# Performance work log

Hardware: AMD Instinct MI355X
Metric: run time of the kernel (lower is better)

## Reference

```python
import jax, jax.numpy as jnp
import numpy as np

N_TASKS = 32
SCALING = 32.0 / 16.0  # lora_alpha / r


def setup_inputs() -> dict:
    key = jax.random.key(0)
    k = jax.random.split(key, 6)
    B_, D_IN, D_OUT, R = 32768, 1024, 1024, 16
    x = jax.random.normal(k[0], (B_, D_IN), dtype=jnp.float32)
    task_ids = jax.random.randint(k[1], (B_,), 0, N_TASKS, dtype=jnp.int32)
    W_base = jax.random.normal(k[2], (D_OUT, D_IN), dtype=jnp.float32) * 0.02
    b_base = jax.random.normal(k[3], (D_OUT,), dtype=jnp.float32) * 0.02
    A = jax.random.normal(k[4], (N_TASKS, R, D_IN), dtype=jnp.float32) * 0.02
    B = jax.random.normal(k[5], (N_TASKS, D_OUT, R), dtype=jnp.float32) * 0.02
    return {"x": x, "task_ids": task_ids, "W_base": W_base, "b_base": b_base, "A": A, "B": B}


def reference(x, task_ids, W_base, b_base, A, B):
    # Base linear: [B, D_in] @ [D_in, D_out] + bias
    result = x @ W_base.T + b_base
    # Per-example task routing. Equivalent to gathering A[t], B[t] per row,
    # expressed as a masked dense contraction over the small task axis.
    onehot = jax.nn.one_hot(task_ids, N_TASKS, dtype=x.dtype)  # [B, T]
    # down-projection for every task, then mask to the selected task: [B, T, r]
    ax = jnp.einsum('bi,tri->btr', x, A) * onehot[:, :, None]
    # up-projection contracting out the task axis: [B, D_out]
    lora_out = jnp.einsum('btr,tor->bo', ax, B) * SCALING
    return result + lora_out
```

## Files before the change

kernel.cpp:

```cpp
#include <hip/hip_runtime.h>


#define D_IN   1024
#define D_OUTV 1024
#define NTASK  32
#define NROWS  32768
#define RLORA  16
#define SCALE  2.0f

typedef unsigned short u16;
typedef __attribute__((ext_vector_type(4))) unsigned short u16x4;
typedef __attribute__((ext_vector_type(8))) unsigned short u16x8;
typedef __attribute__((ext_vector_type(8))) short s16x8;
typedef __attribute__((ext_vector_type(4))) float f32x4;

#define WB_OFF   (0)
#define AB_OFF   (2*1024*1024)
#define BB_OFF   (3*1024*1024)
#define CNT_OFF  (4*1024*1024)
#define RIDX_OFF (CNT_OFF + 512)
#define XG_OFF   (8ull*1024*1024)

__device__ __forceinline__ u16 f2bf(float f) {
  union { float f; unsigned u; } v; v.f = f;
  unsigned r = v.u + 0x7fffu + ((v.u >> 16) & 1u);
  return (u16)(r >> 16);
}

__device__ __forceinline__ void gl2lds16(const void* g, void* s) {
  __builtin_amdgcn_global_load_lds(
      (const __attribute__((address_space(1))) unsigned*)g,
      (__attribute__((address_space(3))) unsigned*)s, 16, 0, 0);
}

__global__ void k_convert(const float* __restrict__ W, const float* __restrict__ A,
                          const float* __restrict__ B, u16* __restrict__ Wb,
                          u16* __restrict__ Ab, u16* __restrict__ Bb) {
  int g = blockIdx.x * blockDim.x + threadIdx.x;
  const int NW = D_OUTV * D_IN / 4;
  const int NA = NTASK * RLORA * D_IN / 4;
  const float* src; u16* dst; int idx;
  if (g < NW) { src = W; dst = Wb; idx = g; }
  else if (g < NW + NA) { src = A; dst = Ab; idx = g - NW; }
  else { src = B; dst = Bb; idx = g - NW - NA; }
  f32x4 v = *(const f32x4*)(src + (size_t)idx * 4);
  u16x4 o;
  o[0] = f2bf(v[0]); o[1] = f2bf(v[1]); o[2] = f2bf(v[2]); o[3] = f2bf(v[3]);
  *(u16x4*)(dst + (size_t)idx * 4) = o;
}

__global__ void k_hist(const int* __restrict__ tasks, int* __restrict__ cnt) {
  __shared__ int h[NTASK];
  int tid = threadIdx.x;
  if (tid < NTASK) h[tid] = 0;
  __syncthreads();
  atomicAdd(&h[tasks[blockIdx.x * 256 + tid]], 1);
  __syncthreads();
  if (tid < NTASK) atomicAdd(&cnt[tid], h[tid]);
}

__global__ void k_scan(int* __restrict__ cnt) {
  int t = threadIdx.x;
  int c = (t < NTASK) ? cnt[t] : 0;
  int v = c;
  for (int d = 1; d < NTASK; d <<= 1) {
    int u = __shfl_up(v, d, 64);
    if (t >= d) v += u;
  }
  if (t < NTASK) {
    int ex = v - c;
    cnt[64 + t] = ex;
    cnt[32 + t] = ex;
    if (t == NTASK - 1) cnt[64 + NTASK] = v;
  }
}

__global__ void k_scatter(const int* __restrict__ tasks, int* __restrict__ cnt,
                          int* __restrict__ ridx) {
  __shared__ int h[NTASK], basev[NTASK];
  int tid = threadIdx.x;
  int b = blockIdx.x * 256 + tid;
  int t = tasks[b];
  if (tid < NTASK) h[tid] = 0;
  __syncthreads();
  atomicAdd(&h[t], 1);
  __syncthreads();
  if (tid < NTASK) {
    basev[tid] = atomicAdd(&cnt[32 + tid], h[tid]);
    h[tid] = 0;
  }
  __syncthreads();
  int r = atomicAdd(&h[t], 1);
  ridx[basev[t] + r] = b;
}

__global__ void k_gatherx(const float* __restrict__ x, const int* __restrict__ ridx,
                          u16* __restrict__ xg) {
  int g = blockIdx.x * 256 + threadIdx.x;
  int pos = g >> 7;
  int c8  = (g & 127) << 3;
  int src = ridx[pos];
  f32x4 a = *(const f32x4*)(x + (size_t)src * D_IN + c8);
  f32x4 b = *(const f32x4*)(x + (size_t)src * D_IN + c8 + 4);
  u16x8 o;
  o[0] = f2bf(a[0]); o[1] = f2bf(a[1]); o[2] = f2bf(a[2]); o[3] = f2bf(a[3]);
  o[4] = f2bf(b[0]); o[5] = f2bf(b[1]); o[6] = f2bf(b[2]); o[7] = f2bf(b[3]);
  *(u16x8*)(xg + (size_t)pos * D_IN + c8) = o;
}

#define BM 128
#define BN 128
#define BK 64
#define NTHR 256
#define SLOTS 3
#define NWG (8 * NTASK * SLOTS)

__global__ __launch_bounds__(NTHR, 3) void k_main_c(
    const u16* __restrict__ xg, const float* __restrict__ bias,
    const u16* __restrict__ Wb, const u16* __restrict__ Ab, const u16* __restrict__ Bb,
    const int* __restrict__ cnt, const int* __restrict__ ridx,
    float* __restrict__ out) {
  __shared__ __align__(16) u16 xs[BM * BK];
  __shared__ __align__(16) u16 wls[BN * BK];
  __shared__ u16 als[RLORA * BK];
  __shared__ u16 axs[BM * 32];
  __shared__ u16 bls[BN * 32];
  __shared__ int rowid_l[BM];

  const int tid = threadIdx.x;
  const int l   = tid & 63;
  const int w   = tid >> 6;
  const int wr  = w >> 1;
  const int wc  = w & 1;
  const int l15 = l & 15;
  const int lg  = l >> 4;

  const int flat = blockIdx.x;
  const int xcd  = flat & 7;
  const int j    = flat >> 3;
  const int cb   = j & 7;
  const int g    = j >> 3;
  const int task = xcd + 8 * (g & 3);
  const int slot = g >> 2;

  const int o0    = cnt[64 + task];
  const int count = cnt[64 + task + 1] - o0;

  for (int s = tid; s < 512; s += NTHR) {
    int c = s >> 2, part = s & 3;
    u16x8 v = {0, 0, 0, 0, 0, 0, 0, 0};
    if (part < 2)
      v = *(const u16x8*)(Bb + ((size_t)(task * D_OUTV) + cb * BN + c) * RLORA + part * 8);
    *(u16x8*)&bls[c * 32 + ((part * 8) ^ ((c & 3) << 3))] = v;
  }
  for (int i = tid; i < BM * 32 / 8; i += NTHR) {
    u16x8 z = {0, 0, 0, 0, 0, 0, 0, 0};
    *(u16x8*)&axs[i * 8] = z;
  }

  for (int chunk = slot; chunk * BM < count; chunk += SLOTS) {
    const int base = chunk * BM;
    __syncthreads();
    if (tid < BM) {
      int s = base + tid;
      rowid_l[tid] = (s < count) ? ridx[o0 + s] : 0;
    }

    f32x4 acc[4][4];
    f32x4 axc0, axc1;
    const f32x4 z4 = {0.f, 0.f, 0.f, 0.f};
    axc0 = z4; axc1 = z4;
#pragma unroll
    for (int m = 0; m < 4; m++)
#pragma unroll
      for (int n = 0; n < 4; n++) acc[m][n] = z4;

    for (int kk = 0; kk < D_IN; kk += BK) {
      __syncthreads();
#pragma unroll
      for (int i = 0; i < 4; i++) {
        int ch = i * NTHR + tid;
        int r = ch >> 3, c = ch & 7;
        int gr = o0 + base + r;
        if (gr > NROWS - 1) gr = NROWS - 1;
        gl2lds16(xg + (size_t)gr * D_IN + kk + ((c ^ (r & 7)) << 3), &xs[ch * 8]);
      }
#pragma unroll
      for (int i = 0; i < 4; i++) {
        int ch = i * NTHR + tid;
        int wrow = ch >> 3, c = ch & 7;
        gl2lds16(Wb + (size_t)(cb * BN + wrow) * D_IN + kk + ((c ^ (wrow & 7)) << 3),
                 &wls[ch * 8]);
      }
      if (tid < 128) {
        int r = tid >> 3, c = tid & 7;
        gl2lds16(Ab + (size_t)(task * RLORA + r) * D_IN + kk + ((c ^ (r & 7)) << 3),
                 &als[tid * 8]);
      }
      __syncthreads();

#pragma unroll
      for (int k0 = 0; k0 < BK; k0 += 32) {
        int kf = k0 + lg * 8;
        s16x8 xf[4], wf[4];
#pragma unroll
        for (int m = 0; m < 4; m++) {
          int row = wr * 64 + m * 16 + l15;
          xf[m] = *(const s16x8*)&xs[row * BK + (kf ^ ((row & 7) << 3))];
        }
#pragma unroll
        for (int n = 0; n < 4; n++) {
          int col = wc * 64 + n * 16 + l15;
          wf[n] = *(const s16x8*)&wls[col * BK + (kf ^ ((col & 7) << 3))];
        }
#pragma unroll
        for (int m = 0; m < 4; m++)
#pragma unroll
          for (int n = 0; n < 4; n++)
            acc[m][n] = __builtin_amdgcn_mfma_f32_16x16x32_bf16(xf[m], wf[n], acc[m][n], 0, 0, 0);
        {
          s16x8 af = *(const s16x8*)&als[l15 * BK + (kf ^ ((l15 & 7) << 3))];
          if (wc == 0) {
            axc0 = __builtin_amdgcn_mfma_f32_16x16x32_bf16(xf[0], af, axc0, 0, 0, 0);
            axc1 = __builtin_amdgcn_mfma_f32_16x16x32_bf16(xf[1], af, axc1, 0, 0, 0);
          } else {
            axc0 = __builtin_amdgcn_mfma_f32_16x16x32_bf16(xf[2], af, axc0, 0, 0, 0);
            axc1 = __builtin_amdgcn_mfma_f32_16x16x32_bf16(xf[3], af, axc1, 0, 0, 0);
          }
        }
      }
    }
    __syncthreads();

#pragma unroll
    for (int i = 0; i < 2; i++) {
#pragma unroll
      for (int j2 = 0; j2 < 4; j2++) {
        int row = wr * 64 + (wc * 2 + i) * 16 + lg * 4 + j2;
        float v = (i == 0) ? axc0[j2] : axc1[j2];
        axs[row * 32 + (l15 ^ ((row & 3) << 3))] = f2bf(v * SCALE);
      }
    }
    __syncthreads();

    int kf2 = lg * 8;
    s16x8 axf[4], blf[4];
#pragma unroll
    for (int m = 0; m < 4; m++) {
      int row = wr * 64 + m * 16 + l15;
      axf[m] = *(const s16x8*)&axs[row * 32 + (kf2 ^ ((row & 3) << 3))];
    }
#pragma unroll
    for (int n = 0; n < 4; n++) {
      int col = wc * 64 + n * 16 + l15;
      blf[n] = *(const s16x8*)&bls[col * 32 + (kf2 ^ ((col & 3) << 3))];
    }
#pragma unroll
    for (int n = 0; n < 4; n++) {
      int colg = cb * BN + wc * 64 + n * 16 + l15;
      float bv = bias[colg];
#pragma unroll
      for (int m = 0; m < 4; m++) {
        f32x4 r = __builtin_amdgcn_mfma_f32_16x16x32_bf16(axf[m], blf[n], acc[m][n], 0, 0, 0);
#pragma unroll
        for (int j2 = 0; j2 < 4; j2++) {
          int lrow = wr * 64 + m * 16 + lg * 4 + j2;
          if (base + lrow < count) {
            int grow = rowid_l[lrow];
            out[(size_t)grow * D_OUTV + colg] = r[j2] + bv;
          }
        }
      }
    }
  }
}

extern "C" void kernel_launch(void* const* d_in, const int* in_sizes, int n_in,
                              void* d_out, int out_size, void* d_ws, size_t ws_size,
                              hipStream_t stream) {
  const float* x     = (const float*)d_in[0];
  const int*   tasks = (const int*)d_in[1];
  const float* W     = (const float*)d_in[2];
  const float* bias  = (const float*)d_in[3];
  const float* A     = (const float*)d_in[4];
  const float* B     = (const float*)d_in[5];
  float* out = (float*)d_out;
  char* ws = (char*)d_ws;
  u16* Wb = (u16*)(ws + WB_OFF);
  u16* Ab = (u16*)(ws + AB_OFF);
  u16* Bb = (u16*)(ws + BB_OFF);
  int* cnt  = (int*)(ws + CNT_OFF);
  int* ridx = (int*)(ws + RIDX_OFF);
  u16* xg   = (u16*)(ws + XG_OFF);

  hipMemsetAsync(cnt, 0, 512, stream);
  k_convert<<<2048, 256, 0, stream>>>(W, A, B, Wb, Ab, Bb);
  k_hist<<<NROWS / 256, 256, 0, stream>>>(tasks, cnt);
  k_scan<<<1, 64, 0, stream>>>(cnt);
  k_scatter<<<NROWS / 256, 256, 0, stream>>>(tasks, cnt, ridx);
  k_gatherx<<<NROWS * D_IN / 8 / 256, 256, 0, stream>>>(x, ridx, xg);
  k_main_c<<<NWG, NTHR, 0, stream>>>(xg, bias, Wb, Ab, Bb, cnt, ridx, out);
}
```

Before: 172.6 us.

## Replace static task/slot mapping with per-XCD atomic work queue

Replaces the fixed mapping of workgroups to (task, column block, slot), where each workgroup strided over its task's chunks by SLOTS, with a dynamic work queue per XCD. Each workgroup claims units through an atomic counter held in the workspace, covering the four tasks assigned to that XCD. This is meant to balance load across workgroups when tasks have uneven row counts and to cut the tail from static striding. In exchange it adds an atomic plus two barriers per unit, and it reloads the B tile for every unit instead of once per workgroup.

```diff
diff --git a/kernel.cpp b/kernel.cpp
--- a/kernel.cpp
+++ b/kernel.cpp
@@ -18,7 +18,7 @@
 #define AB_OFF   (2*1024*1024)
 #define BB_OFF   (3*1024*1024)
 #define CNT_OFF  (4*1024*1024)
-#define RIDX_OFF (CNT_OFF + 512)
+#define RIDX_OFF (CNT_OFF + 1024)
 #define XG_OFF   (8ull*1024*1024)
 
 __device__ __forceinline__ u16 f2bf(float f) {
@@ -112,13 +112,12 @@
 #define BN 128
 #define BK 64
 #define NTHR 256
-#define SLOTS 3
-#define NWG (8 * NTASK * SLOTS)
+#define NWG 768
 
 __global__ __launch_bounds__(NTHR, 3) void k_main_c(
     const u16* __restrict__ xg, const float* __restrict__ bias,
     const u16* __restrict__ Wb, const u16* __restrict__ Ab, const u16* __restrict__ Bb,
-    const int* __restrict__ cnt, const int* __restrict__ ridx,
+    int* __restrict__ cnt, const int* __restrict__ ridx,
     float* __restrict__ out) {
   __shared__ __align__(16) u16 xs[BM * BK];
   __shared__ __align__(16) u16 wls[BN * BK];
@@ -126,6 +125,7 @@
   __shared__ u16 axs[BM * 32];
   __shared__ u16 bls[BN * 32];
   __shared__ int rowid_l[BM];
+  __shared__ int unit_s;
 
   const int tid = threadIdx.x;
   const int l   = tid & 63;
@@ -135,32 +135,46 @@
   const int l15 = l & 15;
   const int lg  = l >> 4;
 
-  const int flat = blockIdx.x;
-  const int xcd  = flat & 7;
-  const int j    = flat >> 3;
-  const int cb   = j & 7;
-  const int g    = j >> 3;
-  const int task = xcd + 8 * (g & 3);
-  const int slot = g >> 2;
-
-  const int o0    = cnt[64 + task];
-  const int count = cnt[64 + task + 1] - o0;
-
-  for (int s = tid; s < 512; s += NTHR) {
-    int c = s >> 2, part = s & 3;
-    u16x8 v = {0, 0, 0, 0, 0, 0, 0, 0};
-    if (part < 2)
-      v = *(const u16x8*)(Bb + ((size_t)(task * D_OUTV) + cb * BN + c) * RLORA + part * 8);
-    *(u16x8*)&bls[c * 32 + ((part * 8) ^ ((c & 3) << 3))] = v;
-  }
+  const int xcd = blockIdx.x & 7;
+
+  const int t0 = xcd, t1 = xcd + 8, t2 = xcd + 16, t3 = xcd + 24;
+  const int o_t0 = cnt[64 + t0], c_t0 = cnt[64 + t0 + 1] - o_t0;
+  const int o_t1 = cnt[64 + t1], c_t1 = cnt[64 + t1 + 1] - o_t1;
+  const int o_t2 = cnt[64 + t2], c_t2 = cnt[64 + t2 + 1] - o_t2;
+  const int o_t3 = cnt[64 + t3], c_t3 = cnt[64 + t3 + 1] - o_t3;
+  const int p1 = (c_t0 + BM - 1) >> 7;
+  const int p2 = p1 + ((c_t1 + BM - 1) >> 7);
+  const int p3 = p2 + ((c_t2 + BM - 1) >> 7);
+  const int myunits = (p3 + ((c_t3 + BM - 1) >> 7)) << 3;
+
   for (int i = tid; i < BM * 32 / 8; i += NTHR) {
     u16x8 z = {0, 0, 0, 0, 0, 0, 0, 0};
     *(u16x8*)&axs[i * 8] = z;
   }
 
-  for (int chunk = slot; chunk * BM < count; chunk += SLOTS) {
-    const int base = chunk * BM;
+  for (;;) {
     __syncthreads();
+    if (tid == 0) unit_s = atomicAdd(&cnt[128 + xcd], 1);
+    __syncthreads();
+    const int u = unit_s;
+    if (u >= myunits) break;
+
+    const int cb   = u & 7;
+    const int cidx = u >> 3;
+    int chunk, o0, count, task;
+    if (cidx < p1)      { chunk = cidx;      o0 = o_t0; count = c_t0; task = t0; }
+    else if (cidx < p2) { chunk = cidx - p1; o0 = o_t1; count = c_t1; task = t1; }
+    else if (cidx < p3) { chunk = cidx - p2; o0 = o_t2; count = c_t2; task = t2; }
+    else                { chunk = cidx - p3; o0 = o_t3; count = c_t3; task = t3; }
+    const int base = chunk << 7;
+
+    for (int s = tid; s < 512; s += NTHR) {
+      int c = s >> 2, part = s & 3;
+      u16x8 v = {0, 0, 0, 0, 0, 0, 0, 0};
+      if (part < 2)
+        v = *(const u16x8*)(Bb + ((size_t)(task * D_OUTV) + cb * BN + c) * RLORA + part * 8);
+      *(u16x8*)&bls[c * 32 + ((part * 8) ^ ((c & 3) << 3))] = v;
+    }
     if (tid < BM) {
       int s = base + tid;
       rowid_l[tid] = (s < count) ? ridx[o0 + s] : 0;
@@ -293,7 +307,7 @@
   int* ridx = (int*)(ws + RIDX_OFF);
   u16* xg   = (u16*)(ws + XG_OFF);
 
-  hipMemsetAsync(cnt, 0, 512, stream);
+  hipMemsetAsync(cnt, 0, 1024, stream);
   k_convert<<<2048, 256, 0, stream>>>(W, A, B, Wb, Ab, Bb);
   k_hist<<<NROWS / 256, 256, 0, stream>>>(tasks, cnt);
   k_scan<<<1, 64, 0, stream>>>(cnt);
```

New measurement: 189.7 us. 9.9% more time.

## Fuse x gather and bf16 conversion into GEMM, merge convert and histogram kernels

Applied to the files above, without the earlier changes.

Drops the separate gather kernel that wrote a bf16 copy of x in task-sorted order. The main GEMM now reads fp32 rows of x directly through the routing indices, converts them to bf16 in registers and stores them into swizzled LDS. The weight-conversion and task-histogram kernels are merged into one launch to save a launch. In exchange, each column-block workgroup re-reads x as fp32, which doubles the bytes per reload versus bf16. The x tile also loses its asynchronous global-to-LDS path, replaced by synchronous register loads before the barrier.

```diff
diff --git a/kernel.cpp b/kernel.cpp
--- a/kernel.cpp
+++ b/kernel.cpp
@@ -19,7 +19,6 @@
 #define BB_OFF   (3*1024*1024)
 #define CNT_OFF  (4*1024*1024)
 #define RIDX_OFF (CNT_OFF + 512)
-#define XG_OFF   (8ull*1024*1024)
 
 __device__ __forceinline__ u16 f2bf(float f) {
   union { float f; unsigned u; } v; v.f = f;
@@ -33,30 +32,32 @@
       (__attribute__((address_space(3))) unsigned*)s, 16, 0, 0);
 }
 
-__global__ void k_convert(const float* __restrict__ W, const float* __restrict__ A,
-                          const float* __restrict__ B, u16* __restrict__ Wb,
-                          u16* __restrict__ Ab, u16* __restrict__ Bb) {
-  int g = blockIdx.x * blockDim.x + threadIdx.x;
-  const int NW = D_OUTV * D_IN / 4;
-  const int NA = NTASK * RLORA * D_IN / 4;
-  const float* src; u16* dst; int idx;
-  if (g < NW) { src = W; dst = Wb; idx = g; }
-  else if (g < NW + NA) { src = A; dst = Ab; idx = g - NW; }
-  else { src = B; dst = Bb; idx = g - NW - NA; }
-  f32x4 v = *(const f32x4*)(src + (size_t)idx * 4);
-  u16x4 o;
-  o[0] = f2bf(v[0]); o[1] = f2bf(v[1]); o[2] = f2bf(v[2]); o[3] = f2bf(v[3]);
-  *(u16x4*)(dst + (size_t)idx * 4) = o;
-}
-
-__global__ void k_hist(const int* __restrict__ tasks, int* __restrict__ cnt) {
-  __shared__ int h[NTASK];
-  int tid = threadIdx.x;
-  if (tid < NTASK) h[tid] = 0;
-  __syncthreads();
-  atomicAdd(&h[tasks[blockIdx.x * 256 + tid]], 1);
-  __syncthreads();
-  if (tid < NTASK) atomicAdd(&cnt[tid], h[tid]);
+__global__ void k_convhist(const float* __restrict__ W, const float* __restrict__ A,
+                           const float* __restrict__ B, const int* __restrict__ tasks,
+                           u16* __restrict__ Wb, u16* __restrict__ Ab,
+                           u16* __restrict__ Bb, int* __restrict__ cnt) {
+  const int bid = blockIdx.x;
+  if (bid < 2048) {
+    int g = bid * 256 + threadIdx.x;
+    const int NW = D_OUTV * D_IN / 4;
+    const int NA = NTASK * RLORA * D_IN / 4;
+    const float* src; u16* dst; int idx;
+    if (g < NW) { src = W; dst = Wb; idx = g; }
+    else if (g < NW + NA) { src = A; dst = Ab; idx = g - NW; }
+    else { src = B; dst = Bb; idx = g - NW - NA; }
+    f32x4 v = *(const f32x4*)(src + (size_t)idx * 4);
+    u16x4 o;
+    o[0] = f2bf(v[0]); o[1] = f2bf(v[1]); o[2] = f2bf(v[2]); o[3] = f2bf(v[3]);
+    *(u16x4*)(dst + (size_t)idx * 4) = o;
+  } else {
+    __shared__ int h[NTASK];
+    int tid = threadIdx.x;
+    if (tid < NTASK) h[tid] = 0;
+    __syncthreads();
+    atomicAdd(&h[tasks[(bid - 2048) * 256 + tid]], 1);
+    __syncthreads();
+    if (tid < NTASK) atomicAdd(&cnt[tid], h[tid]);
+  }
 }
 
 __global__ void k_scan(int* __restrict__ cnt) {
@@ -94,20 +95,6 @@
   ridx[basev[t] + r] = b;
 }
 
-__global__ void k_gatherx(const float* __restrict__ x, const int* __restrict__ ridx,
-                          u16* __restrict__ xg) {
-  int g = blockIdx.x * 256 + threadIdx.x;
-  int pos = g >> 7;
-  int c8  = (g & 127) << 3;
-  int src = ridx[pos];
-  f32x4 a = *(const f32x4*)(x + (size_t)src * D_IN + c8);
-  f32x4 b = *(const f32x4*)(x + (size_t)src * D_IN + c8 + 4);
-  u16x8 o;
-  o[0] = f2bf(a[0]); o[1] = f2bf(a[1]); o[2] = f2bf(a[2]); o[3] = f2bf(a[3]);
-  o[4] = f2bf(b[0]); o[5] = f2bf(b[1]); o[6] = f2bf(b[2]); o[7] = f2bf(b[3]);
-  *(u16x8*)(xg + (size_t)pos * D_IN + c8) = o;
-}
-
 #define BM 128
 #define BN 128
 #define BK 64
@@ -116,7 +103,7 @@
 #define NWG (8 * NTASK * SLOTS)
 
 __global__ __launch_bounds__(NTHR, 3) void k_main_c(
-    const u16* __restrict__ xg, const float* __restrict__ bias,
+    const float* __restrict__ x, const float* __restrict__ bias,
     const u16* __restrict__ Wb, const u16* __restrict__ Ab, const u16* __restrict__ Bb,
     const int* __restrict__ cnt, const int* __restrict__ ridx,
     float* __restrict__ out) {
@@ -165,6 +152,11 @@
       int s = base + tid;
       rowid_l[tid] = (s < count) ? ridx[o0 + s] : 0;
     }
+    __syncthreads();
+
+    int srid[4];
+#pragma unroll
+    for (int i = 0; i < 4; i++) srid[i] = rowid_l[i * 32 + (tid >> 3)];
 
     f32x4 acc[4][4];
     f32x4 axc0, axc1;
@@ -177,14 +169,6 @@
 
     for (int kk = 0; kk < D_IN; kk += BK) {
       __syncthreads();
-#pragma unroll
-      for (int i = 0; i < 4; i++) {
-        int ch = i * NTHR + tid;
-        int r = ch >> 3, c = ch & 7;
-        int gr = o0 + base + r;
-        if (gr > NROWS - 1) gr = NROWS - 1;
-        gl2lds16(xg + (size_t)gr * D_IN + kk + ((c ^ (r & 7)) << 3), &xs[ch * 8]);
-      }
 #pragma unroll
       for (int i = 0; i < 4; i++) {
         int ch = i * NTHR + tid;
@@ -196,6 +180,18 @@
         int r = tid >> 3, c = tid & 7;
         gl2lds16(Ab + (size_t)(task * RLORA + r) * D_IN + kk + ((c ^ (r & 7)) << 3),
                  &als[tid * 8]);
+      }
+#pragma unroll
+      for (int i = 0; i < 4; i++) {
+        int row = i * 32 + (tid >> 3);
+        int k   = (tid & 7) * 8;
+        const float* src = x + (size_t)srid[i] * D_IN + kk + k;
+        f32x4 a = *(const f32x4*)(src);
+        f32x4 b = *(const f32x4*)(src + 4);
+        u16x8 o;
+        o[0] = f2bf(a[0]); o[1] = f2bf(a[1]); o[2] = f2bf(a[2]); o[3] = f2bf(a[3]);
+        o[4] = f2bf(b[0]); o[5] = f2bf(b[1]); o[6] = f2bf(b[2]); o[7] = f2bf(b[3]);
+        *(u16x8*)&xs[row * BK + (k ^ ((row & 7) << 3))] = o;
       }
       __syncthreads();
 
@@ -291,13 +287,10 @@
   u16* Bb = (u16*)(ws + BB_OFF);
   int* cnt  = (int*)(ws + CNT_OFF);
   int* ridx = (int*)(ws + RIDX_OFF);
-  u16* xg   = (u16*)(ws + XG_OFF);
 
   hipMemsetAsync(cnt, 0, 512, stream);
-  k_convert<<<2048, 256, 0, stream>>>(W, A, B, Wb, Ab, Bb);
-  k_hist<<<NROWS / 256, 256, 0, stream>>>(tasks, cnt);
+  k_convhist<<<2176, 256, 0, stream>>>(W, A, B, tasks, Wb, Ab, Bb, cnt);
   k_scan<<<1, 64, 0, stream>>>(cnt);
   k_scatter<<<NROWS / 256, 256, 0, stream>>>(tasks, cnt, ridx);
-  k_gatherx<<<NROWS * D_IN / 8 / 256, 256, 0, stream>>>(x, ridx, xg);
-  k_main_c<<<NWG, NTHR, 0, stream>>>(xg, bias, Wb, Ab, Bb, cnt, ridx, out);
-}
+  k_main_c<<<NWG, NTHR, 0, stream>>>(x, bias, Wb, Ab, Bb, cnt, ridx, out);
+}
```

Result: slower. 194.9 us (+13.0%).
